# Performance work log

Measured on AMD Instinct MI355X. Metric: run time of the kernel, lower is better.

## Reference

```python
import jax, jax.numpy as jnp
import numpy as np

LEAKY_SLOPE = 0.2  # alpha in the torch module
EPS = 1e-10

N_NODES = 100000
N_EDGES = 1600000
IN_F = 128
OUT_F = 64


def setup_inputs() -> dict:
    key = jax.random.key(0)
    k1, k2, k3, k4, k5 = jax.random.split(key, 5)
    h = jax.random.normal(k1, (N_NODES, IN_F), dtype=jnp.float32)
    W = jax.random.normal(k2, (IN_F, OUT_F), dtype=jnp.float32) * (1.0 / np.sqrt(IN_F))
    a1 = jax.random.normal(k3, (OUT_F,), dtype=jnp.float32) * 0.1
    a2 = jax.random.normal(k4, (OUT_F,), dtype=jnp.float32) * 0.1
    edge_index = jax.random.randint(k5, (2, N_EDGES), 0, N_NODES, dtype=jnp.int32)
    return {"h": h, "W": W, "a1": a1, "a2": a2, "edge_index": edge_index}


def reference(h, W, a1, a2, edge_index):
    # h: [N, in_f], W: [in_f, out_f], a1/a2: [out_f], edge_index: [2, E]
    N = h.shape[0]
    Wh = h @ W                                   # [N, out_f]
    row, col = edge_index[0], edge_index[1]      # [E]
    f1 = Wh @ a1                                 # [N]
    f2 = Wh @ a2                                 # [N]
    e = jax.nn.leaky_relu(f1[row] + f2[col], negative_slope=LEAKY_SLOPE)  # [E]
    e_exp = jnp.exp(e - jnp.max(e))              # global-max shift, as in torch code
    exp_sum = jax.ops.segment_sum(e_exp, row, num_segments=N)            # [N]
    alpha = e_exp / (exp_sum[row] + EPS)         # [E]  (dropout is identity in eval)
    weighted_Wh = Wh[col] * alpha[:, None]       # [E, out_f]
    h_prime = jax.ops.segment_sum(weighted_Wh, row, num_segments=N)      # [N, out_f]
    return jax.nn.elu(h_prime)                   # concat=True path
```

## Files before the change

kernel.cpp:

```cpp
#include <hip/hip_runtime.h>
#include <hip/hip_bf16.h>

#define N_NODES 100000
#define N_EDGES 1600000
#define IN_F 128
#define OUT_F 64

#define RPB 64
#define NB  1563
#define C_CHUNKS 250
#define CHUNK 6400
#define M_CNT (NB * C_CHUNKS)
#define SCANA_BLOCKS ((M_CNT + 1023) / 1024)
#define SORT_LDS_CAP 2048

typedef __attribute__((ext_vector_type(8))) short short8;
typedef __attribute__((ext_vector_type(4))) float f32x4;

#define LDS_PITCH 136

__device__ __forceinline__ unsigned short f2bf(float x) {
    unsigned u = __float_as_uint(x);
    return (unsigned short)((u + 0x7FFFu + ((u >> 16) & 1u)) >> 16);
}
__device__ __forceinline__ float bf2f_u(unsigned short b) {
    return __uint_as_float((unsigned)b << 16);
}

__global__ __launch_bounds__(1024) void k_hist(
    const int* __restrict__ ei, int* __restrict__ cnt,
    const float* __restrict__ W, const float* __restrict__ a1,
    const float* __restrict__ a2, float* __restrict__ wa1, float* __restrict__ wa2)
{
    __shared__ int hl[NB];
    const int c = blockIdx.x;
    if (c == C_CHUNKS) {
        const int k = threadIdx.x;
        if (k < IN_F) {
            float s1 = 0.f, s2 = 0.f;
            #pragma unroll 8
            for (int f = 0; f < OUT_F; f++) {
                const float w = W[k * OUT_F + f];
                s1 += w * a1[f];
                s2 += w * a2[f];
            }
            wa1[k] = s1;
            wa2[k] = s2;
        }
        return;
    }
    for (int i = threadIdx.x; i < NB; i += 1024) hl[i] = 0;
    __syncthreads();
    const int e0 = c * CHUNK;
    for (int i = threadIdx.x; i < CHUNK; i += 1024)
        atomicAdd(&hl[ei[e0 + i] >> 6], 1);
    __syncthreads();
    for (int b = threadIdx.x; b < NB; b += 1024)
        cnt[b * C_CHUNKS + c] = hl[b];
}

__global__ __launch_bounds__(256) void k_gemm(
    const float* __restrict__ h, const float* __restrict__ W,
    const float* __restrict__ wa1, const float* __restrict__ wa2,
    unsigned short* __restrict__ Whb, float* __restrict__ f1, float* __restrict__ f2)
{
    __shared__ unsigned short Wt[OUT_F * LDS_PITCH];
    __shared__ unsigned short Al[16 * LDS_PITCH];

    const int tid  = threadIdx.x;
    const int lane = tid & 63;
    const int wav  = tid >> 6;
    const int quad = lane >> 4;
    const int nl   = lane & 15;

    for (int i = tid; i < IN_F * OUT_F; i += 256) {
        const int k = i >> 6, f = i & 63;
        Wt[f * LDS_PITCH + k] = f2bf(W[i]);
    }
    __syncthreads();

    short8 bfrag[4];
    #pragma unroll
    for (int ch = 0; ch < 4; ch++)
        bfrag[ch] = *(const short8*)&Wt[(wav * 16 + nl) * LDS_PITCH + ch * 32 + quad * 8];

    const int srow = tid >> 4;
    const int sc   = tid & 15;
    float w1r[8], w2r[8];
    #pragma unroll
    for (int j = 0; j < 8; j++) { w1r[j] = wa1[sc * 8 + j]; w2r[j] = wa2[sc * 8 + j]; }

    const int ntiles = N_NODES / 16;
    for (int tile = blockIdx.x; tile < ntiles; tile += gridDim.x) {
        const int base = tile * 16;
        __syncthreads();

        const float4 v0 = *(const float4*)&h[(base + srow) * IN_F + sc * 8];
        const float4 v1 = *(const float4*)&h[(base + srow) * IN_F + sc * 8 + 4];
        float p1 = v0.x * w1r[0] + v0.y * w1r[1] + v0.z * w1r[2] + v0.w * w1r[3]
                 + v1.x * w1r[4] + v1.y * w1r[5] + v1.z * w1r[6] + v1.w * w1r[7];
        float p2 = v0.x * w2r[0] + v0.y * w2r[1] + v0.z * w2r[2] + v0.w * w2r[3]
                 + v1.x * w2r[4] + v1.y * w2r[5] + v1.z * w2r[6] + v1.w * w2r[7];
        #pragma unroll
        for (int m = 8; m >= 1; m >>= 1) {
            p1 += __shfl_xor(p1, m, 64);
            p2 += __shfl_xor(p2, m, 64);
        }
        if (sc == 0) { f1[base + srow] = p1; f2[base + srow] = p2; }

        uint4 packed;
        packed.x = (unsigned)f2bf(v0.x) | ((unsigned)f2bf(v0.y) << 16);
        packed.y = (unsigned)f2bf(v0.z) | ((unsigned)f2bf(v0.w) << 16);
        packed.z = (unsigned)f2bf(v1.x) | ((unsigned)f2bf(v1.y) << 16);
        packed.w = (unsigned)f2bf(v1.z) | ((unsigned)f2bf(v1.w) << 16);
        *(uint4*)&Al[srow * LDS_PITCH + sc * 8] = packed;

        __syncthreads();

        f32x4 acc = {0.f, 0.f, 0.f, 0.f};
        #pragma unroll
        for (int ch = 0; ch < 4; ch++) {
            const short8 afrag = *(const short8*)&Al[nl * LDS_PITCH + ch * 32 + quad * 8];
            acc = __builtin_amdgcn_mfma_f32_16x16x32_bf16(afrag, bfrag[ch], acc, 0, 0, 0);
        }

        const int col = wav * 16 + nl;
        #pragma unroll
        for (int r = 0; r < 4; r++)
            Whb[(base + quad * 4 + r) * OUT_F + col] = f2bf(acc[r]);
    }
}

__global__ __launch_bounds__(256) void k_scanA(const int* __restrict__ cnt,
                                               int* __restrict__ bsum)
{
    __shared__ int sd[256];
    const int t = threadIdx.x;
    const int i0 = blockIdx.x * 1024 + t * 4;
    int s = 0;
    #pragma unroll
    for (int k = 0; k < 4; k++) {
        const int i = i0 + k;
        s += (i < M_CNT) ? cnt[i] : 0;
    }
    sd[t] = s; __syncthreads();
    for (int off = 128; off >= 1; off >>= 1) {
        if (t < off) sd[t] += sd[t + off];
        __syncthreads();
    }
    if (t == 0) bsum[blockIdx.x] = sd[0];
}

__global__ __launch_bounds__(256) void k_scanC(int* __restrict__ cnt,
                                               const int* __restrict__ bsum)
{
    __shared__ int red[256];
    __shared__ int ts[256];
    const int t = threadIdx.x;

    int pv = 0;
    for (int i = t; i < (int)blockIdx.x; i += 256) pv += bsum[i];
    red[t] = pv; __syncthreads();
    for (int off = 128; off >= 1; off >>= 1) {
        if (t < off) red[t] += red[t + off];
        __syncthreads();
    }
    const int bpref = red[0];

    const int i0 = blockIdx.x * 1024 + t * 4;
    int v[4]; int s = 0;
    #pragma unroll
    for (int k = 0; k < 4; k++) {
        const int i = i0 + k;
        v[k] = (i < M_CNT) ? cnt[i] : 0;
        s += v[k];
    }
    ts[t] = s; __syncthreads();
    for (int off = 1; off < 256; off <<= 1) {
        const int x = (t >= off) ? ts[t - off] : 0;
        __syncthreads();
        ts[t] += x;
        __syncthreads();
    }
    int excl = ts[t] - s + bpref;
    #pragma unroll
    for (int k = 0; k < 4; k++) {
        const int i = i0 + k;
        if (i < M_CNT) cnt[i] = excl;
        excl += v[k];
    }
}

__global__ __launch_bounds__(1024) void k_scatter(
    const int* __restrict__ ei,
    const float* __restrict__ f1,
    const float* __restrict__ f2,
    const int* __restrict__ cnt,
    uint2* __restrict__ pairs)
{
    __shared__ int cur[NB];
    const int c = blockIdx.x;
    for (int b = threadIdx.x; b < NB; b += 1024)
        cur[b] = cnt[b * C_CHUNKS + c];
    __syncthreads();

    const int e0 = c * CHUNK;
    for (int i = threadIdx.x; i < CHUNK; i += 1024) {
        const int r  = ei[e0 + i];
        const int cl = ei[N_EDGES + e0 + i];
        float x = f1[r] + f2[cl];
        x = (x >= 0.f) ? x : 0.2f * x;
        const float ee = __expf(x);
        const int pos = atomicAdd(&cur[r >> 6], 1);
        pairs[pos] = make_uint2(((unsigned)(r & 63) << 17) | (unsigned)cl,
                                __float_as_uint(ee));
    }
}

__global__ __launch_bounds__(256) void k_sort(
    const int* __restrict__ cnt,
    const uint2* __restrict__ pairs,
    uint2* __restrict__ pairs2,
    int* __restrict__ rowptr)
{
    __shared__ uint2 sp[SORT_LDS_CAP];
    __shared__ int cnt64[64];
    __shared__ int cur64[64];

    const int b   = blockIdx.x;
    const int tid = threadIdx.x;
    const int start = cnt[b * C_CHUNKS];
    const int end   = (b == NB - 1) ? N_EDGES : cnt[(b + 1) * C_CHUNKS];
    const int len   = end - start;

    if (tid < 64) cnt64[tid] = 0;
    __syncthreads();

    for (int i = tid; i < len; i += 256) {
        const uint2 p = pairs[start + i];
        if (i < SORT_LDS_CAP) sp[i] = p;
        atomicAdd(&cnt64[p.x >> 17], 1);
    }
    __syncthreads();

    if (tid < 64) {
        const int v = cnt64[tid];
        int s = v;
        #pragma unroll
        for (int off = 1; off < 64; off <<= 1) {
            const int x = __shfl_up(s, off, 64);
            if (tid >= off) s += x;
        }
        cur64[tid] = s - v;
        const int g = b * 64 + tid;
        if (g < N_NODES) rowptr[g] = start + s - v;
    }
    __syncthreads();

    for (int i = tid; i < len; i += 256) {
        const uint2 p = (i < SORT_LDS_CAP) ? sp[i] : pairs[start + i];
        const int pos = atomicAdd(&cur64[p.x >> 17], 1);
        pairs2[start + pos] = p;
    }
    if (b == 0 && tid == 0) rowptr[N_NODES] = N_EDGES;
}

__global__ __launch_bounds__(256) void k_agg(
    const int* __restrict__ rowptr,
    const uint2* __restrict__ pairs2,
    const unsigned short* __restrict__ Whb,
    float* __restrict__ out)
{
    const int wid  = (blockIdx.x * 256 + threadIdx.x) >> 6;
    const int lane = threadIdx.x & 63;
    if (wid >= N_NODES) return;

    const int start = rowptr[wid];
    const int end   = rowptr[wid + 1];
    const int deg   = end - start;

    if (deg <= 0) {
        out[wid * OUT_F + lane] = 0.f;
        return;
    }

    const int nb = (deg + 7) >> 3;

    float acc = 0.f, s = 0.f;
    uint2 p[8];

    #pragma unroll
    for (int k = 0; k < 8; k++) {
        const int idx = start + k;
        p[k] = pairs2[(idx < end) ? idx : (end - 1)];
    }

    int j = start;
    for (int b = 1; b < nb; b++) {
        const int jn = start + b * 8;
        uint2 q[8];
        #pragma unroll
        for (int k = 0; k < 8; k++) {
            const int idx = jn + k;
            q[k] = pairs2[(idx < end) ? idx : (end - 1)];
        }
        float wh[8];
        #pragma unroll
        for (int k = 0; k < 8; k++)
            wh[k] = bf2f_u(Whb[(((int)(p[k].x & 0x1FFFFu)) << 6) + lane]);
        #pragma unroll
        for (int k = 0; k < 8; k++) {
            const float ee = (j + k < end) ? __uint_as_float(p[k].y) : 0.f;
            acc += ee * wh[k];
            s   += ee;
        }
        #pragma unroll
        for (int k = 0; k < 8; k++) p[k] = q[k];
        j = jn;
    }

    {
        float wh[8];
        #pragma unroll
        for (int k = 0; k < 8; k++)
            wh[k] = bf2f_u(Whb[(((int)(p[k].x & 0x1FFFFu)) << 6) + lane]);
        #pragma unroll
        for (int k = 0; k < 8; k++) {
            const float ee = (j + k < end) ? __uint_as_float(p[k].y) : 0.f;
            acc += ee * wh[k];
            s   += ee;
        }
    }

    const float r = acc / (s + 1e-10f);
    out[wid * OUT_F + lane] = (r > 0.f) ? r : expm1f(r);
}

extern "C" void kernel_launch(void* const* d_in, const int* in_sizes, int n_in,
                              void* d_out, int out_size, void* d_ws, size_t ws_size,
                              hipStream_t stream) {
    const float* h  = (const float*)d_in[0];
    const float* W  = (const float*)d_in[1];
    const float* a1 = (const float*)d_in[2];
    const float* a2 = (const float*)d_in[3];
    const int* ei   = (const int*)d_in[4];
    float* out      = (float*)d_out;

    float* ws = (float*)d_ws;
    unsigned short* Whb = (unsigned short*)ws;
    float* f1     = ws + 3200000;
    float* f2     = f1 + N_NODES;
    float* wa1    = f2 + N_NODES;
    float* wa2    = wa1 + 128;
    int*   cnt    = (int*)(wa2 + 128);
    int*   bsum   = cnt + M_CNT;
    int*   rowptr = bsum + 384;
    int*   pad    = rowptr + 100002;
    if ((size_t)(pad - (int*)ws) & 1) pad++;
    uint2* pairs  = (uint2*)pad;
    uint2* pairs2 = pairs + N_EDGES;

    k_hist   <<<C_CHUNKS + 1, 1024, 0, stream>>>(ei, cnt, W, a1, a2, wa1, wa2);
    k_scanA  <<<SCANA_BLOCKS, 256, 0, stream>>>(cnt, bsum);
    k_scanC  <<<SCANA_BLOCKS, 256, 0, stream>>>(cnt, bsum);
    k_gemm   <<<1250, 256, 0, stream>>>(h, W, wa1, wa2, Whb, f1, f2);
    k_scatter<<<C_CHUNKS, 1024, 0, stream>>>(ei, f1, f2, cnt, pairs);
    k_sort   <<<NB, 256, 0, stream>>>(cnt, pairs, pairs2, rowptr);
    k_agg    <<<(N_NODES * 64 + 255) / 256, 256, 0, stream>>>(rowptr, pairs2, Whb, out);
}
```

Baseline: 247.1 us.

## Process two nodes per wave in aggregation and four tiles per GEMM iteration

The aggregation kernel now gives each wavefront two consecutive destination nodes and interleaves their edge loops in chunks of four, so more independent gathers are in flight per wave and half as many waves are launched. Tails use scalar loops instead of clamped padded loads. The GEMM kernel stages four 16-row tiles in LDS per barrier pair, which cuts synchronisation per tile, and launches fewer blocks. The risk is lower occupancy and divergence when the two nodes have different degrees, plus extra LDS use in the GEMM.

```diff
diff --git a/kernel.cpp b/kernel.cpp
--- a/kernel.cpp
+++ b/kernel.cpp
@@ -13,6 +13,7 @@
 #define M_CNT (NB * C_CHUNKS)
 #define SCANA_BLOCKS ((M_CNT + 1023) / 1024)
 #define SORT_LDS_CAP 2048
+#define NTILES (N_NODES / 16)
 
 typedef __attribute__((ext_vector_type(8))) short short8;
 typedef __attribute__((ext_vector_type(4))) float f32x4;
@@ -65,7 +66,7 @@
     unsigned short* __restrict__ Whb, float* __restrict__ f1, float* __restrict__ f2)
 {
     __shared__ unsigned short Wt[OUT_F * LDS_PITCH];
-    __shared__ unsigned short Al[16 * LDS_PITCH];
+    __shared__ unsigned short Al[64 * LDS_PITCH];
 
     const int tid  = threadIdx.x;
     const int lane = tid & 63;
@@ -90,44 +91,57 @@
     #pragma unroll
     for (int j = 0; j < 8; j++) { w1r[j] = wa1[sc * 8 + j]; w2r[j] = wa2[sc * 8 + j]; }
 
-    const int ntiles = N_NODES / 16;
-    for (int tile = blockIdx.x; tile < ntiles; tile += gridDim.x) {
-        const int base = tile * 16;
-        __syncthreads();
-
-        const float4 v0 = *(const float4*)&h[(base + srow) * IN_F + sc * 8];
-        const float4 v1 = *(const float4*)&h[(base + srow) * IN_F + sc * 8 + 4];
-        float p1 = v0.x * w1r[0] + v0.y * w1r[1] + v0.z * w1r[2] + v0.w * w1r[3]
-                 + v1.x * w1r[4] + v1.y * w1r[5] + v1.z * w1r[6] + v1.w * w1r[7];
-        float p2 = v0.x * w2r[0] + v0.y * w2r[1] + v0.z * w2r[2] + v0.w * w2r[3]
-                 + v1.x * w2r[4] + v1.y * w2r[5] + v1.z * w2r[6] + v1.w * w2r[7];
-        #pragma unroll
-        for (int m = 8; m >= 1; m >>= 1) {
-            p1 += __shfl_xor(p1, m, 64);
-            p2 += __shfl_xor(p2, m, 64);
-        }
-        if (sc == 0) { f1[base + srow] = p1; f2[base + srow] = p2; }
-
-        uint4 packed;
-        packed.x = (unsigned)f2bf(v0.x) | ((unsigned)f2bf(v0.y) << 16);
-        packed.y = (unsigned)f2bf(v0.z) | ((unsigned)f2bf(v0.w) << 16);
-        packed.z = (unsigned)f2bf(v1.x) | ((unsigned)f2bf(v1.y) << 16);
-        packed.w = (unsigned)f2bf(v1.z) | ((unsigned)f2bf(v1.w) << 16);
-        *(uint4*)&Al[srow * LDS_PITCH + sc * 8] = packed;
-
-        __syncthreads();
-
-        f32x4 acc = {0.f, 0.f, 0.f, 0.f};
-        #pragma unroll
-        for (int ch = 0; ch < 4; ch++) {
-            const short8 afrag = *(const short8*)&Al[nl * LDS_PITCH + ch * 32 + quad * 8];
-            acc = __builtin_amdgcn_mfma_f32_16x16x32_bf16(afrag, bfrag[ch], acc, 0, 0, 0);
-        }
-
-        const int col = wav * 16 + nl;
-        #pragma unroll
-        for (int r = 0; r < 4; r++)
-            Whb[(base + quad * 4 + r) * OUT_F + col] = f2bf(acc[r]);
+    const int ngroups = (NTILES + 3) / 4;
+    for (int g = blockIdx.x; g < ngroups; g += gridDim.x) {
+        __syncthreads();
+
+        #pragma unroll
+        for (int sub = 0; sub < 4; sub++) {
+            const int tile = g * 4 + sub;
+            if (tile < NTILES) {
+                const int base = tile * 16;
+                const float4 v0 = *(const float4*)&h[(base + srow) * IN_F + sc * 8];
+                const float4 v1 = *(const float4*)&h[(base + srow) * IN_F + sc * 8 + 4];
+                float p1 = v0.x * w1r[0] + v0.y * w1r[1] + v0.z * w1r[2] + v0.w * w1r[3]
+                         + v1.x * w1r[4] + v1.y * w1r[5] + v1.z * w1r[6] + v1.w * w1r[7];
+                float p2 = v0.x * w2r[0] + v0.y * w2r[1] + v0.z * w2r[2] + v0.w * w2r[3]
+                         + v1.x * w2r[4] + v1.y * w2r[5] + v1.z * w2r[6] + v1.w * w2r[7];
+                #pragma unroll
+                for (int m = 8; m >= 1; m >>= 1) {
+                    p1 += __shfl_xor(p1, m, 64);
+                    p2 += __shfl_xor(p2, m, 64);
+                }
+                if (sc == 0) { f1[base + srow] = p1; f2[base + srow] = p2; }
+
+                uint4 packed;
+                packed.x = (unsigned)f2bf(v0.x) | ((unsigned)f2bf(v0.y) << 16);
+                packed.y = (unsigned)f2bf(v0.z) | ((unsigned)f2bf(v0.w) << 16);
+                packed.z = (unsigned)f2bf(v1.x) | ((unsigned)f2bf(v1.y) << 16);
+                packed.w = (unsigned)f2bf(v1.z) | ((unsigned)f2bf(v1.w) << 16);
+                *(uint4*)&Al[(sub * 16 + srow) * LDS_PITCH + sc * 8] = packed;
+            }
+        }
+
+        __syncthreads();
+
+        #pragma unroll
+        for (int sub = 0; sub < 4; sub++) {
+            const int tile = g * 4 + sub;
+            if (tile < NTILES) {
+                const int base = tile * 16;
+                f32x4 acc = {0.f, 0.f, 0.f, 0.f};
+                #pragma unroll
+                for (int ch = 0; ch < 4; ch++) {
+                    const short8 afrag = *(const short8*)
+                        &Al[(sub * 16 + nl) * LDS_PITCH + ch * 32 + quad * 8];
+                    acc = __builtin_amdgcn_mfma_f32_16x16x32_bf16(afrag, bfrag[ch], acc, 0, 0, 0);
+                }
+                const int col = wav * 16 + nl;
+                #pragma unroll
+                for (int r = 0; r < 4; r++)
+                    Whb[(base + quad * 4 + r) * OUT_F + col] = f2bf(acc[r]);
+            }
+        }
     }
 }
 
@@ -271,69 +285,88 @@
     const unsigned short* __restrict__ Whb,
     float* __restrict__ out)
 {
-    const int wid  = (blockIdx.x * 256 + threadIdx.x) >> 6;
+    const int w    = (blockIdx.x * 256 + threadIdx.x) >> 6;
     const int lane = threadIdx.x & 63;
-    if (wid >= N_NODES) return;
-
-    const int start = rowptr[wid];
-    const int end   = rowptr[wid + 1];
-    const int deg   = end - start;
-
-    if (deg <= 0) {
-        out[wid * OUT_F + lane] = 0.f;
-        return;
-    }
-
-    const int nb = (deg + 7) >> 3;
-
-    float acc = 0.f, s = 0.f;
-    uint2 p[8];
-
-    #pragma unroll
-    for (int k = 0; k < 8; k++) {
-        const int idx = start + k;
-        p[k] = pairs2[(idx < end) ? idx : (end - 1)];
-    }
-
-    int j = start;
-    for (int b = 1; b < nb; b++) {
-        const int jn = start + b * 8;
-        uint2 q[8];
-        #pragma unroll
-        for (int k = 0; k < 8; k++) {
-            const int idx = jn + k;
-            q[k] = pairs2[(idx < end) ? idx : (end - 1)];
-        }
-        float wh[8];
-        #pragma unroll
-        for (int k = 0; k < 8; k++)
+    const int n0   = w * 2;
+    if (n0 >= N_NODES) return;
+    const int n1   = n0 + 1;
+
+    const int s0 = rowptr[n0];
+    const int e0 = rowptr[n0 + 1];
+    const int e1 = rowptr[n0 + 2];
+
+    float acc0 = 0.f, ss0 = 0.f, acc1 = 0.f, ss1 = 0.f;
+    int j0 = s0, j1 = e0;
+
+    while (j0 + 4 <= e0 && j1 + 4 <= e1) {
+        uint2 p0[4], p1[4];
+        #pragma unroll
+        for (int k = 0; k < 4; k++) p0[k] = pairs2[j0 + k];
+        #pragma unroll
+        for (int k = 0; k < 4; k++) p1[k] = pairs2[j1 + k];
+        float wh0[4], wh1[4];
+        #pragma unroll
+        for (int k = 0; k < 4; k++)
+            wh0[k] = bf2f_u(Whb[(((int)(p0[k].x & 0x1FFFFu)) << 6) + lane]);
+        #pragma unroll
+        for (int k = 0; k < 4; k++)
+            wh1[k] = bf2f_u(Whb[(((int)(p1[k].x & 0x1FFFFu)) << 6) + lane]);
+        #pragma unroll
+        for (int k = 0; k < 4; k++) {
+            const float a = __uint_as_float(p0[k].y);
+            const float bb = __uint_as_float(p1[k].y);
+            acc0 += a * wh0[k];  ss0 += a;
+            acc1 += bb * wh1[k]; ss1 += bb;
+        }
+        j0 += 4; j1 += 4;
+    }
+
+    for (; j0 + 4 <= e0; j0 += 4) {
+        uint2 p[4];
+        #pragma unroll
+        for (int k = 0; k < 4; k++) p[k] = pairs2[j0 + k];
+        float wh[4];
+        #pragma unroll
+        for (int k = 0; k < 4; k++)
             wh[k] = bf2f_u(Whb[(((int)(p[k].x & 0x1FFFFu)) << 6) + lane]);
         #pragma unroll
-        for (int k = 0; k < 8; k++) {
-            const float ee = (j + k < end) ? __uint_as_float(p[k].y) : 0.f;
-            acc += ee * wh[k];
-            s   += ee;
-        }
-        #pragma unroll
-        for (int k = 0; k < 8; k++) p[k] = q[k];
-        j = jn;
-    }
-
-    {
-        float wh[8];
-        #pragma unroll
-        for (int k = 0; k < 8; k++)
+        for (int k = 0; k < 4; k++) {
+            const float a = __uint_as_float(p[k].y);
+            acc0 += a * wh[k]; ss0 += a;
+        }
+    }
+    for (; j0 < e0; j0++) {
+        const uint2 p = pairs2[j0];
+        const float a = __uint_as_float(p.y);
+        acc0 += a * bf2f_u(Whb[(((int)(p.x & 0x1FFFFu)) << 6) + lane]);
+        ss0  += a;
+    }
+
+    for (; j1 + 4 <= e1; j1 += 4) {
+        uint2 p[4];
+        #pragma unroll
+        for (int k = 0; k < 4; k++) p[k] = pairs2[j1 + k];
+        float wh[4];
+        #pragma unroll
+        for (int k = 0; k < 4; k++)
             wh[k] = bf2f_u(Whb[(((int)(p[k].x & 0x1FFFFu)) << 6) + lane]);
         #pragma unroll
-        for (int k = 0; k < 8; k++) {
-            const float ee = (j + k < end) ? __uint_as_float(p[k].y) : 0.f;
-            acc += ee * wh[k];
-            s   += ee;
-        }
-    }
-
-    const float r = acc / (s + 1e-10f);
-    out[wid * OUT_F + lane] = (r > 0.f) ? r : expm1f(r);
+        for (int k = 0; k < 4; k++) {
+            const float a = __uint_as_float(p[k].y);
+            acc1 += a * wh[k]; ss1 += a;
+        }
+    }
+    for (; j1 < e1; j1++) {
+        const uint2 p = pairs2[j1];
+        const float a = __uint_as_float(p.y);
+        acc1 += a * bf2f_u(Whb[(((int)(p.x & 0x1FFFFu)) << 6) + lane]);
+        ss1  += a;
+    }
+
+    float r0 = acc0 / (ss0 + 1e-10f);
+    float r1 = acc1 / (ss1 + 1e-10f);
+    out[n0 * OUT_F + lane] = (r0 > 0.f) ? r0 : expm1f(r0);
+    out[n1 * OUT_F + lane] = (r1 > 0.f) ? r1 : expm1f(r1);
 }
 
 extern "C" void kernel_launch(void* const* d_in, const int* in_sizes, int n_in,
@@ -363,8 +396,8 @@
     k_hist   <<<C_CHUNKS + 1, 1024, 0, stream>>>(ei, cnt, W, a1, a2, wa1, wa2);
     k_scanA  <<<SCANA_BLOCKS, 256, 0, stream>>>(cnt, bsum);
     k_scanC  <<<SCANA_BLOCKS, 256, 0, stream>>>(cnt, bsum);
-    k_gemm   <<<1250, 256, 0, stream>>>(h, W, wa1, wa2, Whb, f1, f2);
+    k_gemm   <<<782, 256, 0, stream>>>(h, W, wa1, wa2, Whb, f1, f2);
     k_scatter<<<C_CHUNKS, 1024, 0, stream>>>(ei, f1, f2, cnt, pairs);
     k_sort   <<<NB, 256, 0, stream>>>(cnt, pairs, pairs2, rowptr);
-    k_agg    <<<(N_NODES * 64 + 255) / 256, 256, 0, stream>>>(rowptr, pairs2, Whb, out);
-}
+    k_agg    <<<(N_NODES / 2 * 64 + 255) / 256, 256, 0, stream>>>(rowptr, pairs2, Whb, out);
+}
```

New measurement: 229.5 us (median of 3 runs). 1.08x faster.
